# Kernel optimization log

Hardware: AMD Instinct MI355X
Metric: run time of the kernel (lower is better)

## Reference

```python
import jax, jax.numpy as jnp
import numpy as np

D = 1024
W_SIZE = 512
K_ENGRAMS = 16
REPEAT = W_SIZE // K_ENGRAMS  # 32
LN_EPS = 1e-5


def setup_inputs() -> dict:
    key = jax.random.key(0)
    ks = jax.random.split(key, 6)
    B, NW = 4, 16
    engrams = jax.random.normal(ks[0], (B, NW, K_ENGRAMS, D), dtype=jnp.float32)
    pos_emb = 0.02 * jax.random.normal(ks[1], (1, 1, W_SIZE, D), dtype=jnp.float32)
    w1 = 0.02 * jax.random.normal(ks[2], (D, D), dtype=jnp.float32)
    b1 = jnp.zeros((D,), dtype=jnp.float32)
    w2 = 0.02 * jax.random.normal(ks[3], (D, D), dtype=jnp.float32)
    b2 = jnp.zeros((D,), dtype=jnp.float32)
    gamma = jnp.ones((D,), dtype=jnp.float32)
    beta = jnp.zeros((D,), dtype=jnp.float32)
    return {"engrams": engrams, "pos_emb": pos_emb, "w1": w1, "b1": b1,
            "w2": w2, "b2": b2, "gamma": gamma, "beta": beta}


def reference(engrams, pos_emb, w1, b1, w2, b2, gamma, beta):
    # (B, nw, K, d) -> (B, nw, W, d) via repeat_interleave along axis 2
    x = jnp.repeat(engrams, REPEAT, axis=2) + pos_emb
    # refine MLP: Linear -> GELU (exact) -> Linear, with residual
    h = jax.nn.gelu(jnp.einsum('bnwd,de->bnwe', x, w1.T) + b1, approximate=False)
    x = x + jnp.einsum('bnwd,de->bnwe', h, w2.T) + b2
    # LayerNorm over last dim
    mu = jnp.mean(x, axis=-1, keepdims=True)
    var = jnp.mean(jnp.square(x - mu), axis=-1, keepdims=True)
    return (x - mu) * jax.lax.rsqrt(var + LN_EPS) * gamma + beta
```

## Files before the change

### kernel.cpp

```cpp
#include <hip/hip_runtime.h>
#include <hip/hip_bf16.h>
#include <math.h>

#define D_DIM 1024
#define NROWS 32768
#define NE_ROWS 1024
#define A1_ROWS 1536
#define NT2 32

typedef __attribute__((ext_vector_type(8))) short bf16x8;
typedef __attribute__((ext_vector_type(4))) float f32x4;

static __device__ __forceinline__ ushort f2bf(float f) {
  union { float f; unsigned u; } un; un.f = f;
  unsigned u = un.u;
  unsigned r = u + 0x7fffu + ((u >> 16) & 1u);
  return (ushort)(r >> 16);
}
static __device__ __forceinline__ float bf2f(ushort h) {
  union { unsigned u; float f; } un; un.u = ((unsigned)h) << 16;
  return un.f;
}
static __device__ __forceinline__ float gelu_exact(float v) {
  return 0.5f * v * (1.0f + erff(v * 0.70710678118654752f));
}

__global__ void cast_all_kernel(const float* __restrict__ w1, const float* __restrict__ w2,
                                const float* __restrict__ eng, const float* __restrict__ pos,
                                ushort* __restrict__ dst) {
  int i = blockIdx.x * blockDim.x + threadIdx.x;
  float4 v;
  if (i < 262144) v = ((const float4*)w1)[i];
  else if (i < 524288) v = ((const float4*)w2)[i - 262144];
  else if (i < 786432) v = ((const float4*)eng)[i - 524288];
  else v = ((const float4*)pos)[i - 786432];
  ushort4 o;
  o.x = f2bf(v.x); o.y = f2bf(v.y); o.z = f2bf(v.z); o.w = f2bf(v.w);
  ((ushort4*)dst)[i] = o;
}

__global__ __launch_bounds__(256) void packB_kernel(const ushort* __restrict__ w2b,
                                                    ushort* __restrict__ pack) {
  int id = blockIdx.x * 256 + threadIdx.x;
  int l = id & 63;
  int n = (id >> 6) & 3;
  int kt = (id >> 8) & 31;
  int wcnt = id >> 13;
  int c = (wcnt >> 1) * 128 + (wcnt & 1) * 64 + n * 16 + (l & 15);
  int k = kt * 32 + (l >> 4) * 8;
  bf16x8 v = *(const bf16x8*)(w2b + ((size_t)c << 10) + k);
  *(bf16x8*)(pack + ((size_t)id << 3)) = v;
}

__global__ __launch_bounds__(256) void gemm_bt(const ushort* __restrict__ A,
                                               const ushort* __restrict__ B,
                                               float* __restrict__ C,
                                               int M, int N, int K,
                                               const float* __restrict__ bias,
                                               int biasRow0) {
  __shared__ ushort sA[128 * 64];
  __shared__ ushort sB[128 * 64];

  int nwg = gridDim.x;
  int bid = blockIdx.x;
  if ((nwg & 7) == 0) {
    int cpx = nwg >> 3;
    bid = (bid & 7) * cpx + (bid >> 3);
  }
  int ntn = N >> 7;
  int mt = bid / ntn, nt = bid % ntn;
  int brow = mt << 7, bcol = nt << 7;

  int tid = threadIdx.x;
  int wv = tid >> 6, lane = tid & 63;
  int wm = (wv >> 1) << 6, wn = (wv & 1) << 6;
  int lr = lane & 15, lk = lane >> 4;
  int srow = lane >> 3;
  int scolsw = (((lane & 7) ^ ((lane >> 3) & 7)) << 3);

  f32x4 acc[4][4];
#pragma unroll
  for (int m = 0; m < 4; ++m)
#pragma unroll
    for (int n = 0; n < 4; ++n) acc[m][n] = (f32x4){0.f, 0.f, 0.f, 0.f};

  for (int k0 = 0; k0 < K; k0 += 64) {
    __syncthreads();
#pragma unroll
    for (int j = 0; j < 4; ++j) {
      int c = (wv << 2) + j;
      int row = (c << 3) + srow;
      const ushort* gA = A + (brow + row) * K + k0 + scolsw;
      const ushort* gB = B + (bcol + row) * K + k0 + scolsw;
      __builtin_amdgcn_global_load_lds(
          (const __attribute__((address_space(1))) unsigned int*)gA,
          (__attribute__((address_space(3))) unsigned int*)&sA[c << 9], 16, 0, 0);
      __builtin_amdgcn_global_load_lds(
          (const __attribute__((address_space(1))) unsigned int*)gB,
          (__attribute__((address_space(3))) unsigned int*)&sB[c << 9], 16, 0, 0);
    }
    __syncthreads();
#pragma unroll
    for (int kk = 0; kk < 2; ++kk) {
      int rdoff = (((kk << 2) | lk) ^ (lr & 7)) << 3;
      bf16x8 af[4], bfr[4];
#pragma unroll
      for (int m = 0; m < 4; ++m)
        af[m] = *(const bf16x8*)&sA[(wm + (m << 4) + lr) * 64 + rdoff];
#pragma unroll
      for (int n = 0; n < 4; ++n)
        bfr[n] = *(const bf16x8*)&sB[(wn + (n << 4) + lr) * 64 + rdoff];
#pragma unroll
      for (int m = 0; m < 4; ++m)
#pragma unroll
        for (int n = 0; n < 4; ++n)
          acc[m][n] = __builtin_amdgcn_mfma_f32_16x16x32_bf16(af[m], bfr[n], acc[m][n], 0, 0, 0);
    }
  }

#pragma unroll
  for (int m = 0; m < 4; ++m)
#pragma unroll
    for (int n = 0; n < 4; ++n)
#pragma unroll
      for (int i = 0; i < 4; ++i) {
        int row = brow + wm + (m << 4) + (lk << 2) + i;
        int col = bcol + wn + (n << 4) + lr;
        float v = acc[m][n][i];
        if (row >= biasRow0) v += bias[col];
        C[(long)row * N + col] = v;
      }
}

__global__ __launch_bounds__(256) void gelu_kernel(const float* __restrict__ xw1,
                                                   ushort* __restrict__ h) {
  int r = blockIdx.x;
  int t = threadIdx.x;
  int bn = r >> 9;
  int w = r & 511;
  int er = bn * 16 + (w >> 5);
  float4 e = ((const float4*)(xw1 + er * D_DIM))[t];
  float4 p = ((const float4*)(xw1 + (NE_ROWS + w) * D_DIM))[t];
  ushort4 o;
  o.x = f2bf(gelu_exact(e.x + p.x));
  o.y = f2bf(gelu_exact(e.y + p.y));
  o.z = f2bf(gelu_exact(e.z + p.z));
  o.w = f2bf(gelu_exact(e.w + p.w));
  ((ushort4*)(h + (long)r * D_DIM))[t] = o;
}

__global__ __launch_bounds__(256, 4) void gemm2_128(const ushort* __restrict__ A,
                                                    const ushort* __restrict__ BP,
                                                    ushort* __restrict__ Y) {
  __shared__ ushort sA[2][4096];
  const int K = 1024;

  int bid = blockIdx.x;
  int x = bid & 7, jj = bid >> 3;
  int mt = (x << 5) + (jj >> 3);
  int nt = jj & 7;
  long brow = (long)mt << 7;
  int bcol = nt << 7;

  int tid = threadIdx.x;
  int wv = tid >> 6, l = tid & 63;
  int wr = wv >> 1, wc = wv & 1;
  int lr = l & 15, lk = l >> 4;

  int srow0 = (wv << 4) + (l >> 2);
  int slog = (((l & 3) ^ ((l >> 3) & 3)) << 3);
  const ushort* aS = A + (brow + srow0) * (long)K + slog;

  int rdswz = (lk ^ ((lr >> 1) & 3)) << 3;
  int aO = (((wr << 6) + lr) << 5) + rdswz;

  const ushort* bP = BP + (((size_t)((nt << 1) | wc)) << 16) + (l << 3);

  f32x4 acc[4][4];
#pragma unroll
  for (int m = 0; m < 4; ++m)
#pragma unroll
    for (int n = 0; n < 4; ++n) acc[m][n] = (f32x4){0.f, 0.f, 0.f, 0.f};

#define STG(kt) do {                                                                 \
    int p_ = (kt) & 1; int ko_ = (kt) << 5;                                          \
    _Pragma("unroll")                                                                \
    for (int j2 = 0; j2 < 2; ++j2) {                                                 \
      __builtin_amdgcn_global_load_lds(                                              \
        (const __attribute__((address_space(1))) unsigned int*)(aS + ko_ + (long)(j2 << 6) * K), \
        (__attribute__((address_space(3))) unsigned int*)&sA[p_][(j2 << 11) + (wv << 9)], 16, 0, 0); \
    } } while (0)

#define LDB(BUF, kt) do {                                                            \
    _Pragma("unroll")                                                                \
    for (int n = 0; n < 4; ++n)                                                      \
      BUF[n] = *(const bf16x8*)(bP + ((((kt) << 2) | n) << 9));                      \
    __builtin_amdgcn_sched_barrier(0);                                               \
  } while (0)

#define BAR asm volatile("s_barrier" ::: "memory")

  bf16x8 bA[4], bB[4];

  STG(0);
  __builtin_amdgcn_sched_barrier(0);
  LDB(bA, 0);
  STG(1);
  asm volatile("s_waitcnt vmcnt(2)" ::: "memory");
  BAR;

#define STEP(t, BU, BL) do {                                                         \
    if ((t) + 1 < NT2) LDB(BL, (t) + 1);            \
    bf16x8 af[4];                                                                    \
    _Pragma("unroll")                                                                \
    for (int m = 0; m < 4; ++m) af[m] = *(const bf16x8*)&sA[(t) & 1][aO + (m << 9)]; \
    __builtin_amdgcn_s_setprio(1);                                                   \
    _Pragma("unroll")                                                                \
    for (int m = 0; m < 4; ++m)                                                      \
      _Pragma("unroll")                                                              \
      for (int n = 0; n < 4; ++n)                                                    \
        acc[m][n] = __builtin_amdgcn_mfma_f32_16x16x32_bf16(af[m], BU[n], acc[m][n], 0, 0, 0); \
    __builtin_amdgcn_s_setprio(0);                                                   \
    if ((t) < NT2 - 1) {                                                             \
      BAR;                                        \
      if ((t) + 2 < NT2) {                                                           \
        STG((t) + 2);                                                                \
        asm volatile("s_waitcnt vmcnt(2)" ::: "memory");   \
      } else {                                                                       \
        asm volatile("s_waitcnt vmcnt(0)" ::: "memory");             \
      }                                                                              \
      BAR;                                                                           \
    }                                                                                \
  } while (0)

  for (int t = 0; t < NT2; t += 2) {
    STEP(t, bA, bB);
    STEP(t + 1, bB, bA);
  }
#undef STEP
#undef STG
#undef LDB
#undef BAR

#pragma unroll
  for (int m = 0; m < 4; ++m)
#pragma unroll
    for (int n = 0; n < 4; ++n) {
      int col = bcol + (wc << 6) + (n << 4) + lr;
#pragma unroll
      for (int i = 0; i < 4; ++i) {
        long row = brow + (wr << 6) + (m << 4) + (lk << 2) + i;
        Y[(row << 11) + col] = f2bf(acc[m][n][i]);
      }
    }
}

__global__ __launch_bounds__(256) void ln_kernel(const float* __restrict__ eng,
                                                 const float* __restrict__ pos,
                                                 const float* __restrict__ b2,
                                                 const float* __restrict__ gamma,
                                                 const float* __restrict__ beta,
                                                 float* __restrict__ out) {
  __shared__ float red[8];
  int r = blockIdx.x;
  int t = threadIdx.x;
  int bn = r >> 9, w = r & 511;
  int er = bn * 16 + (w >> 5);
  float4 xe = ((const float4*)(eng + er * D_DIM))[t];
  float4 xp = ((const float4*)(pos + w * D_DIM))[t];
  ushort4 yv = ((const ushort4*)((const ushort*)out + ((size_t)r << 11)))[t];
  float4 bb = ((const float4*)b2)[t];
  float v0 = xe.x + xp.x + bf2f(yv.x) + bb.x;
  float v1 = xe.y + xp.y + bf2f(yv.y) + bb.y;
  float v2 = xe.z + xp.z + bf2f(yv.z) + bb.z;
  float v3 = xe.w + xp.w + bf2f(yv.w) + bb.w;
  float s  = v0 + v1 + v2 + v3;
  float sq = v0 * v0 + v1 * v1 + v2 * v2 + v3 * v3;
  int lane = t & 63, wv = t >> 6;
#pragma unroll
  for (int off = 32; off > 0; off >>= 1) {
    s  += __shfl_down(s, off);
    sq += __shfl_down(sq, off);
  }
  if (lane == 0) { red[wv] = s; red[4 + wv] = sq; }
  __syncthreads();
  float S  = red[0] + red[1] + red[2] + red[3];
  float SQ = red[4] + red[5] + red[6] + red[7];
  float mu = S * (1.0f / 1024.0f);
  float var = SQ * (1.0f / 1024.0f) - mu * mu;
  float rs = rsqrtf(var + 1e-5f);
  float4 g = ((const float4*)gamma)[t];
  float4 bt = ((const float4*)beta)[t];
  float4 o;
  o.x = (v0 - mu) * rs * g.x + bt.x;
  o.y = (v1 - mu) * rs * g.y + bt.y;
  o.z = (v2 - mu) * rs * g.z + bt.z;
  o.w = (v3 - mu) * rs * g.w + bt.w;
  ((float4*)(out + ((size_t)r << 10)))[t] = o;
}

extern "C" void kernel_launch(void* const* d_in, const int* in_sizes, int n_in,
                              void* d_out, int out_size, void* d_ws, size_t ws_size,
                              hipStream_t stream) {
  const float* eng   = (const float*)d_in[0];
  const float* pos   = (const float*)d_in[1];
  const float* w1    = (const float*)d_in[2];
  const float* b1    = (const float*)d_in[3];
  const float* w2    = (const float*)d_in[4];
  const float* b2    = (const float*)d_in[5];
  const float* gamma = (const float*)d_in[6];
  const float* beta  = (const float*)d_in[7];
  float* out = (float*)d_out;

  char* ws = (char*)d_ws;
  ushort* w1b = (ushort*)(ws);
  ushort* w2b = (ushort*)(ws + (2u << 20));
  ushort* a1b = (ushort*)(ws + (4u << 20));
  float*  xw1 = (float*)(ws + (7u << 20));
  ushort* hb  = (ushort*)(ws + (13u << 20));
  ushort* bpk = (ushort*)(ws + (77u << 20));

  cast_all_kernel<<<3584, 256, 0, stream>>>(w1, w2, eng, pos, w1b);

  packB_kernel<<<512, 256, 0, stream>>>(w2b, bpk);

  gemm_bt<<<(A1_ROWS / 128) * (D_DIM / 128), 256, 0, stream>>>(a1b, w1b, xw1,
                                                               A1_ROWS, D_DIM, D_DIM,
                                                               b1, NE_ROWS);

  gelu_kernel<<<NROWS, 256, 0, stream>>>(xw1, hb);

  gemm2_128<<<2048, 256, 0, stream>>>(hb, bpk, (ushort*)out);

  ln_kernel<<<NROWS, 256, 0, stream>>>(eng, pos, b2, gamma, beta, out);
}
```

Measured before the change: 173.5 us.

## Pack GELU output into MFMA fragment layout and stream A directly from global

The GELU kernel now writes its bf16 output already arranged in the per-lane MFMA A-fragment order, and the second GEMM loads A fragments straight from global memory into registers instead of staging through LDS with barriers. This removes LDS traffic, swizzling and the two barriers per k-step, and uses a simple register double-buffer. The cost is that every wave reads its A fragments from global/L2 with no LDS sharing across the two column waves, and occupancy is lowered to 3 blocks per CU, so more L2 bandwidth is needed.

Result: no change. 175.9 us (+1.4%).

```diff
diff --git a/kernel.cpp b/kernel.cpp
--- a/kernel.cpp
+++ b/kernel.cpp
@@ -132,29 +132,35 @@
       }
 }
 
-__global__ __launch_bounds__(256) void gelu_kernel(const float* __restrict__ xw1,
-                                                   ushort* __restrict__ h) {
-  int r = blockIdx.x;
-  int t = threadIdx.x;
-  int bn = r >> 9;
-  int w = r & 511;
+__global__ __launch_bounds__(256) void gelu_pack(const float* __restrict__ xw1,
+                                                 ushort* __restrict__ hp) {
+  int sid = blockIdx.x * 256 + threadIdx.x;
+  int l = sid & 63;
+  int frag = sid >> 6;
+  int kt = frag & 31, rg = frag >> 5;
+  int row = (rg << 4) + (l & 15);
+  int bn = row >> 9, w = row & 511;
   int er = bn * 16 + (w >> 5);
-  float4 e = ((const float4*)(xw1 + er * D_DIM))[t];
-  float4 p = ((const float4*)(xw1 + (NE_ROWS + w) * D_DIM))[t];
-  ushort4 o;
-  o.x = f2bf(gelu_exact(e.x + p.x));
-  o.y = f2bf(gelu_exact(e.y + p.y));
-  o.z = f2bf(gelu_exact(e.z + p.z));
-  o.w = f2bf(gelu_exact(e.w + p.w));
-  ((ushort4*)(h + (long)r * D_DIM))[t] = o;
-}
-
-__global__ __launch_bounds__(256, 4) void gemm2_128(const ushort* __restrict__ A,
-                                                    const ushort* __restrict__ BP,
-                                                    ushort* __restrict__ Y) {
-  __shared__ ushort sA[2][4096];
-  const int K = 1024;
-
+  int kb = (kt << 5) + ((l >> 4) << 3);
+  const float* e = xw1 + ((size_t)er << 10) + kb;
+  const float* p = xw1 + ((size_t)(NE_ROWS + w) << 10) + kb;
+  float4 e0 = *(const float4*)e, e1 = *(const float4*)(e + 4);
+  float4 p0 = *(const float4*)p, p1 = *(const float4*)(p + 4);
+  bf16x8 o;
+  o[0] = (short)f2bf(gelu_exact(e0.x + p0.x));
+  o[1] = (short)f2bf(gelu_exact(e0.y + p0.y));
+  o[2] = (short)f2bf(gelu_exact(e0.z + p0.z));
+  o[3] = (short)f2bf(gelu_exact(e0.w + p0.w));
+  o[4] = (short)f2bf(gelu_exact(e1.x + p1.x));
+  o[5] = (short)f2bf(gelu_exact(e1.y + p1.y));
+  o[6] = (short)f2bf(gelu_exact(e1.z + p1.z));
+  o[7] = (short)f2bf(gelu_exact(e1.w + p1.w));
+  *(bf16x8*)(hp + ((size_t)sid << 3)) = o;
+}
+
+__global__ __launch_bounds__(256, 3) void gemm2_stream(const ushort* __restrict__ AP,
+                                                       const ushort* __restrict__ BP,
+                                                       ushort* __restrict__ Y) {
   int bid = blockIdx.x;
   int x = bid & 7, jj = bid >> 3;
   int mt = (x << 5) + (jj >> 3);
@@ -167,13 +173,7 @@
   int wr = wv >> 1, wc = wv & 1;
   int lr = l & 15, lk = l >> 4;
 
-  int srow0 = (wv << 4) + (l >> 2);
-  int slog = (((l & 3) ^ ((l >> 3) & 3)) << 3);
-  const ushort* aS = A + (brow + srow0) * (long)K + slog;
-
-  int rdswz = (lk ^ ((lr >> 1) & 3)) << 3;
-  int aO = (((wr << 6) + lr) << 5) + rdswz;
-
+  const ushort* aP = AP + (((size_t)((mt << 3) + (wr << 2)) << 5) << 9) + (l << 3);
   const ushort* bP = BP + (((size_t)((nt << 1) | wc)) << 16) + (l << 3);
 
   f32x4 acc[4][4];
@@ -182,65 +182,36 @@
 #pragma unroll
     for (int n = 0; n < 4; ++n) acc[m][n] = (f32x4){0.f, 0.f, 0.f, 0.f};
 
-#define STG(kt) do {                                                                 \
-    int p_ = (kt) & 1; int ko_ = (kt) << 5;                                          \
+#define LDA(BUF, kt) do {                                                            \
     _Pragma("unroll")                                                                \
-    for (int j2 = 0; j2 < 2; ++j2) {                                                 \
-      __builtin_amdgcn_global_load_lds(                                              \
-        (const __attribute__((address_space(1))) unsigned int*)(aS + ko_ + (long)(j2 << 6) * K), \
-        (__attribute__((address_space(3))) unsigned int*)&sA[p_][(j2 << 11) + (wv << 9)], 16, 0, 0); \
-    } } while (0)
-
+    for (int m = 0; m < 4; ++m)                                                      \
+      BUF[m] = *(const bf16x8*)(aP + (((m << 5) | (kt)) << 9));                      \
+  } while (0)
 #define LDB(BUF, kt) do {                                                            \
     _Pragma("unroll")                                                                \
     for (int n = 0; n < 4; ++n)                                                      \
       BUF[n] = *(const bf16x8*)(bP + ((((kt) << 2) | n) << 9));                      \
-    __builtin_amdgcn_sched_barrier(0);                                               \
   } while (0)
-
-#define BAR asm volatile("s_barrier" ::: "memory")
-
-  bf16x8 bA[4], bB[4];
-
-  STG(0);
-  __builtin_amdgcn_sched_barrier(0);
-  LDB(bA, 0);
-  STG(1);
-  asm volatile("s_waitcnt vmcnt(2)" ::: "memory");
-  BAR;
-
-#define STEP(t, BU, BL) do {                                                         \
-    if ((t) + 1 < NT2) LDB(BL, (t) + 1);            \
-    bf16x8 af[4];                                                                    \
-    _Pragma("unroll")                                                                \
-    for (int m = 0; m < 4; ++m) af[m] = *(const bf16x8*)&sA[(t) & 1][aO + (m << 9)]; \
-    __builtin_amdgcn_s_setprio(1);                                                   \
+#define MFMA16(AF, BF)                                                               \
     _Pragma("unroll")                                                                \
     for (int m = 0; m < 4; ++m)                                                      \
       _Pragma("unroll")                                                              \
       for (int n = 0; n < 4; ++n)                                                    \
-        acc[m][n] = __builtin_amdgcn_mfma_f32_16x16x32_bf16(af[m], BU[n], acc[m][n], 0, 0, 0); \
-    __builtin_amdgcn_s_setprio(0);                                                   \
-    if ((t) < NT2 - 1) {                                                             \
-      BAR;                                        \
-      if ((t) + 2 < NT2) {                                                           \
-        STG((t) + 2);                                                                \
-        asm volatile("s_waitcnt vmcnt(2)" ::: "memory");   \
-      } else {                                                                       \
-        asm volatile("s_waitcnt vmcnt(0)" ::: "memory");             \
-      }                                                                              \
-      BAR;                                                                           \
-    }                                                                                \
-  } while (0)
-
+        acc[m][n] = __builtin_amdgcn_mfma_f32_16x16x32_bf16(AF[m], BF[n], acc[m][n], 0, 0, 0)
+
+  bf16x8 a0[4], a1[4], b0[4], b1[4];
+  LDA(a0, 0); LDB(b0, 0);
   for (int t = 0; t < NT2; t += 2) {
-    STEP(t, bA, bB);
-    STEP(t + 1, bB, bA);
+    int t1 = (t + 1 < NT2) ? t + 1 : t;
+    LDA(a1, t1); LDB(b1, t1);
+    MFMA16(a0, b0);
+    int t2 = (t + 2 < NT2) ? t + 2 : t;
+    LDA(a0, t2); LDB(b0, t2);
+    MFMA16(a1, b1);
   }
-#undef STEP
-#undef STG
+#undef LDA
 #undef LDB
-#undef BAR
+#undef MFMA16
 
 #pragma unroll
   for (int m = 0; m < 4; ++m)
@@ -317,7 +288,7 @@
   ushort* w2b = (ushort*)(ws + (2u << 20));
   ushort* a1b = (ushort*)(ws + (4u << 20));
   float*  xw1 = (float*)(ws + (7u << 20));
-  ushort* hb  = (ushort*)(ws + (13u << 20));
+  ushort* hp  = (ushort*)(ws + (13u << 20));
   ushort* bpk = (ushort*)(ws + (77u << 20));
 
   cast_all_kernel<<<3584, 256, 0, stream>>>(w1, w2, eng, pos, w1b);
@@ -328,9 +299,9 @@
                                                                A1_ROWS, D_DIM, D_DIM,
                                                                b1, NE_ROWS);
 
-  gelu_kernel<<<NROWS, 256, 0, stream>>>(xw1, hb);
-
-  gemm2_128<<<2048, 256, 0, stream>>>(hb, bpk, (ushort*)out);
+  gelu_pack<<<16384, 256, 0, stream>>>(xw1, hp);
+
+  gemm2_stream<<<2048, 256, 0, stream>>>(hp, bpk, (ushort*)out);
 
   ln_kernel<<<NROWS, 256, 0, stream>>>(eng, pos, b2, gamma, beta, out);
 }
```
